# Kernel optimization log

Hardware: AMD Instinct MI355X
Metric: run time of the kernel (lower is better)

## Reference

```python
import jax, jax.numpy as jnp
import numpy as np

B, N, D = 8, 512, 16


def setup_inputs() -> dict:
    key = jax.random.key(0)
    k1, k2 = jax.random.split(key)
    # Fully-connected adjacency with diagonal = -1 (self is excluded as neighbor),
    # matching the tf.where(adj != -1) -> reshape [-1, N, N-1] pattern.
    adj_matrix = jnp.where(jnp.eye(N, dtype=bool)[None, :, :], -1, 1)
    adj_matrix = jnp.broadcast_to(adj_matrix, (B, N, N)).astype(jnp.int64)
    adj_coef = jax.random.normal(k1, (B, N, N), dtype=jnp.float32)
    neighbour_messages = jax.random.normal(k2, (B, N, D), dtype=jnp.float32)
    return {
        "adj_matrix": adj_matrix,
        "adj_coef": adj_coef,
        "neighbour_messages": neighbour_messages,
    }


def reference(adj_matrix, adj_coef, neighbour_messages):
    b, n, d = neighbour_messages.shape
    # tf.where(adj != -1) enumerates, per row i (in ascending column order), the
    # N-1 valid neighbor columns. Reproduce jit-safely: push invalid cols to the
    # end with sentinel n, sort, keep first n-1.
    cols = jnp.arange(n)[None, None, :]
    valid = adj_matrix != -1
    neighbor_idx = jnp.sort(jnp.where(valid, cols, n), axis=-1)[..., : n - 1]  # [B,N,N-1]
    # Batched gather: [B,N,N-1,D]
    gathered = neighbour_messages[jnp.arange(b)[:, None, None], neighbor_idx]
    # Concat self features with neighbor features along the 'slot' axis -> [B,N,N,D]
    updated = jnp.concatenate([neighbour_messages[:, :, None, :], gathered], axis=2)
    # Weight each slot by its adjacency coefficient, then flatten slots*features.
    updated = adj_coef[..., None] * updated
    return updated.reshape(b, n, n * d)
```

## Files before the change

kernel.cpp:

```cpp
#include <hip/hip_runtime.h>

#define NN 512
#define DD 16

typedef __attribute__((ext_vector_type(4))) float f32x4;

__global__ __launch_bounds__(512) void graph_layer_kernel(
    const int*    __restrict__ adj,
    const float*  __restrict__ coef,
    const float4* __restrict__ msg4,
    float4*       __restrict__ out4)
{
    __shared__ float scoef[NN];
    __shared__ int   snb[NN];
    __shared__ int   wtot[8];

    const int row  = blockIdx.x;
    const int b    = row >> 9;
    const int i    = row & (NN - 1);
    const int t    = threadIdx.x;
    const int lane = t & 63;
    const int wv   = t >> 6;

    scoef[t] = coef[(size_t)row * NN + t];

    const int  a     = adj[(size_t)row * NN + t];
    const bool valid = (a != -1);
    const unsigned long long m = __ballot(valid);
    const int  rank  = __popcll(m & ((1ULL << lane) - 1ULL));
    snb[t] = NN - 1;
    if (lane == 0) wtot[wv] = __popcll(m);
    __syncthreads();

    int base = 0;
    #pragma unroll
    for (int w = 0; w < 8; ++w)
        base += (w < wv) ? wtot[w] : 0;
    if (valid) {
        const int pos = base + rank;
        if (pos < NN) snb[pos] = t;
    }
    __syncthreads();

    const float4* mb   = msg4 + (size_t)b * (NN * 4);
    float4*       orow = out4 + (size_t)row * (NN * 4);
    #pragma unroll
    for (int k = 0; k < 4; ++k) {
        const int g = t + k * 512;
        const int j = g >> 2;
        const int q = g & 3;
        const int s = (j == 0) ? i : snb[j - 1];
        const float c = scoef[j];
        const float4 v = mb[s * 4 + q];
        f32x4 o = { c * v.x, c * v.y, c * v.z, c * v.w };
        __builtin_nontemporal_store(o, (f32x4*)&orow[g]);
    }
}

extern "C" void kernel_launch(void* const* d_in, const int* in_sizes, int n_in,
                              void* d_out, int out_size, void* d_ws, size_t ws_size,
                              hipStream_t stream) {
    const int*    adj  = (const int*)d_in[0];
    const float*  coef = (const float*)d_in[1];
    const float4* msg4 = (const float4*)d_in[2];
    float4*       out4 = (float4*)d_out;

    const int B = 8;
    graph_layer_kernel<<<B * NN, 512, 0, stream>>>(adj, coef, msg4, out4);
}
```

Baseline: 160.5 us.

## Split neighbor compaction and output expansion into separate kernels via workspace

Computes compacted neighbor indices in a first kernel and stores them to workspace, then a flat grid-strided expand kernel gathers messages, scales by coefficients and writes the output. This decouples the ballot/scan and barriers from the bandwidth-bound store phase and uses smaller blocks. It adds an extra launch and a round-trip of an index array the size of the adjacency matrix through global memory. It falls back to the fused kernel if workspace is insufficient.

Result: slower. 170.6 us (+6.3%).

```diff
diff --git a/kernel.cpp b/kernel.cpp
--- a/kernel.cpp
+++ b/kernel.cpp
@@ -4,6 +4,63 @@
 #define DD 16
 
 typedef __attribute__((ext_vector_type(4))) float f32x4;
+
+__global__ __launch_bounds__(512) void compact_kernel(
+    const int* __restrict__ adj,
+    int*       __restrict__ nbw)
+{
+    __shared__ int snb[NN];
+    __shared__ int wtot[8];
+
+    const int row  = blockIdx.x;
+    const int t    = threadIdx.x;
+    const int lane = t & 63;
+    const int wv   = t >> 6;
+
+    const int  a     = adj[(size_t)row * NN + t];
+    const bool valid = (a != -1);
+    const unsigned long long m = __ballot(valid);
+    const int  rank  = __popcll(m & ((1ULL << lane) - 1ULL));
+    snb[t] = NN - 1;
+    if (lane == 0) wtot[wv] = __popcll(m);
+    __syncthreads();
+
+    int base = 0;
+    #pragma unroll
+    for (int w = 0; w < 8; ++w)
+        base += (w < wv) ? wtot[w] : 0;
+    if (valid) {
+        const int pos = base + rank;
+        if (pos < NN) snb[pos] = t;
+    }
+    __syncthreads();
+
+    nbw[(size_t)row * NN + t] = snb[t];
+}
+
+__global__ __launch_bounds__(256) void expand_kernel(
+    const int*    __restrict__ nbw,
+    const float*  __restrict__ coef,
+    const float4* __restrict__ msg4,
+    float4*       __restrict__ out4)
+{
+    const unsigned tid = blockIdx.x * 256u + threadIdx.x;
+    #pragma unroll
+    for (int k = 0; k < 8; ++k) {
+        const unsigned g   = tid + (unsigned)k * (4096u * 256u);
+        const unsigned row = g >> 11;
+        const unsigned r   = g & 2047u;
+        const unsigned j   = r >> 2;
+        const unsigned q   = r & 3u;
+        const unsigned b   = row >> 9;
+        const unsigned i   = row & 511u;
+        const unsigned s   = (j == 0) ? i : (unsigned)nbw[row * 512u + (j - 1)];
+        const float    c   = coef[row * 512u + j];
+        const float4   v   = msg4[(b << 11) + (s << 2) + q];
+        f32x4 o = { c * v.x, c * v.y, c * v.z, c * v.w };
+        __builtin_nontemporal_store(o, (f32x4*)&out4[g]);
+    }
+}
 
 __global__ __launch_bounds__(512) void graph_layer_kernel(
     const int*    __restrict__ adj,
@@ -66,5 +123,13 @@
     float4*       out4 = (float4*)d_out;
 
     const int B = 8;
-    graph_layer_kernel<<<B * NN, 512, 0, stream>>>(adj, coef, msg4, out4);
+    const size_t ws_needed = (size_t)B * NN * NN * sizeof(int);
+
+    if (ws_size >= ws_needed && d_ws != nullptr) {
+        int* nbw = (int*)d_ws;
+        compact_kernel<<<B * NN, 512, 0, stream>>>(adj, nbw);
+        expand_kernel<<<4096, 256, 0, stream>>>(nbw, coef, msg4, out4);
+    } else {
+        graph_layer_kernel<<<B * NN, 512, 0, stream>>>(adj, coef, msg4, out4);
+    }
 }
```

## Process four rows per block, drop nontemporal stores and shared coef staging

Applied to the files above, without the earlier changes.

Each block now handles four output rows. It computes the neighbor compaction for all four before a single pair of barriers, then streams the outputs row by row. Coefficients are read directly from global memory instead of being staged in LDS. The store order within each row is rotated by row phase. Nontemporal stores are replaced with ordinary stores, and the grid shrinks by a factor of four. This amortizes launch and sync overhead at the cost of more registers and fewer blocks, and the change of store cache policy may shift write-bandwidth behavior.

Result: slower. 165.1 us (+2.9%).

```diff
diff --git a/kernel.cpp b/kernel.cpp
--- a/kernel.cpp
+++ b/kernel.cpp
@@ -1,7 +1,7 @@
 #include <hip/hip_runtime.h>
 
-#define NN 512
-#define DD 16
+#define NN  512
+#define RPB 4
 
 typedef __attribute__((ext_vector_type(4))) float f32x4;
 
@@ -11,49 +11,62 @@
     const float4* __restrict__ msg4,
     float4*       __restrict__ out4)
 {
-    __shared__ float scoef[NN];
-    __shared__ int   snb[NN];
-    __shared__ int   wtot[8];
+    __shared__ int snb[RPB][NN];
+    __shared__ int wtot[RPB][8];
 
-    const int row  = blockIdx.x;
-    const int b    = row >> 9;
-    const int i    = row & (NN - 1);
+    const int row0 = blockIdx.x * RPB;
     const int t    = threadIdx.x;
     const int lane = t & 63;
     const int wv   = t >> 6;
+    const int b    = row0 >> 9;
 
-    scoef[t] = coef[(size_t)row * NN + t];
-
-    const int  a     = adj[(size_t)row * NN + t];
-    const bool valid = (a != -1);
-    const unsigned long long m = __ballot(valid);
-    const int  rank  = __popcll(m & ((1ULL << lane) - 1ULL));
-    snb[t] = NN - 1;
-    if (lane == 0) wtot[wv] = __popcll(m);
-    __syncthreads();
-
-    int base = 0;
+    unsigned long long m[RPB];
+    int  rank [RPB];
+    bool valid[RPB];
     #pragma unroll
-    for (int w = 0; w < 8; ++w)
-        base += (w < wv) ? wtot[w] : 0;
-    if (valid) {
-        const int pos = base + rank;
-        if (pos < NN) snb[pos] = t;
+    for (int r = 0; r < RPB; ++r) {
+        const int a = adj[(size_t)(row0 + r) * NN + t];
+        valid[r] = (a != -1);
+        m[r]     = __ballot(valid[r]);
+        rank[r]  = __popcll(m[r] & ((1ULL << lane) - 1ULL));
+        snb[r][t] = NN - 1;
+        if (lane == 0) wtot[r][wv] = __popcll(m[r]);
     }
     __syncthreads();
 
-    const float4* mb   = msg4 + (size_t)b * (NN * 4);
-    float4*       orow = out4 + (size_t)row * (NN * 4);
     #pragma unroll
-    for (int k = 0; k < 4; ++k) {
-        const int g = t + k * 512;
-        const int j = g >> 2;
-        const int q = g & 3;
-        const int s = (j == 0) ? i : snb[j - 1];
-        const float c = scoef[j];
-        const float4 v = mb[s * 4 + q];
-        f32x4 o = { c * v.x, c * v.y, c * v.z, c * v.w };
-        __builtin_nontemporal_store(o, (f32x4*)&orow[g]);
+    for (int r = 0; r < RPB; ++r) {
+        int base = 0;
+        #pragma unroll
+        for (int w = 0; w < 8; ++w)
+            base += (w < wv) ? wtot[r][w] : 0;
+        if (valid[r]) {
+            const int pos = base + rank[r];
+            if (pos < NN) snb[r][pos] = t;
+        }
+    }
+    __syncthreads();
+
+    const float4* mb = msg4 + ((size_t)b << 11);
+    #pragma unroll 1
+    for (int r = 0; r < RPB; ++r) {
+        const int    row  = row0 + r;
+        const int    i    = row & (NN - 1);
+        const float* crow = coef + (size_t)row * NN;
+        float4*      orow = out4 + (size_t)row * (NN * 4);
+        const int    ph   = row & 3;
+        #pragma unroll
+        for (int kk = 0; kk < 4; ++kk) {
+            const int k = (kk + ph) & 3;
+            const int g = t + k * 512;
+            const int j = g >> 2;
+            const int q = g & 3;
+            const int s = (j == 0) ? i : snb[r][j - 1];
+            const float  c = crow[j];
+            const float4 v = mb[(s << 2) + q];
+            f32x4 o = { c * v.x, c * v.y, c * v.z, c * v.w };
+            *(f32x4*)&orow[g] = o;
+        }
     }
 }
 
@@ -66,5 +79,5 @@
     float4*       out4 = (float4*)d_out;
 
     const int B = 8;
-    graph_layer_kernel<<<B * NN, 512, 0, stream>>>(adj, coef, msg4, out4);
+    graph_layer_kernel<<<(B * NN) / RPB, 512, 0, stream>>>(adj, coef, msg4, out4);
 }
```
